# Performance work log

Hardware: AMD Instinct MI355X
Metric: run time of the kernel (lower is better)

## Reference

```python
import jax, jax.numpy as jnp
import numpy as np

B, SQ, SK, H, HK, D = 2, 2048, 2048, 32, 8, 128

def setup_inputs() -> dict:
    key = jax.random.key(0)
    k1, k2, k3 = jax.random.split(key, 3)
    q = jax.random.normal(k1, (B, SQ, H, D), dtype=jnp.float32)
    kv = jax.random.normal(k2, (B, SK, 2, HK, D), dtype=jnp.float32)
    # ragged valid lengths per batch (True = keep)
    lengths = jax.random.randint(k3, (B,), SK // 2, SK + 1)
    key_padding_mask = jnp.arange(SK)[None, :] < lengths[:, None]
    return {"q": q, "kv": kv, "key_padding_mask": key_padding_mask}

def reference(q, kv, key_padding_mask):
    b, sq, h, d = q.shape
    sk, hk = kv.shape[1], kv.shape[3]
    if hk != h:
        kv = jnp.repeat(kv, h // hk, axis=3)  # GQA: (hkv g) contiguous repeat
    k, v = kv[:, :, 0], kv[:, :, 1]  # (B, Sk, H, D)
    scale = 1.0 / jnp.sqrt(jnp.asarray(d, dtype=q.dtype))
    scores = jnp.einsum('bthd,bshd->bhts', q, k * scale)  # (B, H, Sq, Sk)
    pad = jnp.where(key_padding_mask, 0.0, -10000.0).astype(scores.dtype)
    scores = scores + pad[:, None, None, :]
    row = jnp.arange(sq)[:, None]
    col = jnp.arange(sk)[None, :]
    sk_valid = key_padding_mask.sum(-1)[:, None, None, None]  # (B,1,1,1)
    causal_mask = col[None, None] > row[None, None] + sk_valid - sq
    scores = jnp.where(causal_mask, jnp.asarray(-10000.0, scores.dtype), scores)
    attention = jax.nn.softmax(scores, axis=-1)
    # dropout p=0.0 -> identity
    return jnp.einsum('bhts,bshd->bthd', attention, v)  # (B, Sq, H, D)
```

## Files before the change

### kernel.cpp

```cpp
#include <hip/hip_runtime.h>
#include <hip/hip_bf16.h>
#include <cstdint>
#include <cstddef>

constexpr int B_ = 2, SQ_ = 2048, SK_ = 2048, H_ = 32, HK_ = 8, D_ = 128;
constexpr float SCALE_ = 0.08838834764831845f;

typedef __attribute__((ext_vector_type(4))) float f32x4;
typedef __attribute__((ext_vector_type(8))) short bf16x8;
typedef __attribute__((ext_vector_type(4))) short bf16x4;

__device__ __forceinline__ unsigned short f2bf(float f) {
  union { float f; uint32_t u; } v; v.f = f;
  uint32_t u = v.u;
  return (unsigned short)((u + 0x7FFFu + ((u >> 16) & 1u)) >> 16);
}

__device__ __forceinline__ void gload16(const void* g, void* l) {
  __builtin_amdgcn_global_load_lds((const __attribute__((address_space(1))) void*)g,
                                   (__attribute__((address_space(3))) void*)l, 16, 0, 0);
}

__device__ __forceinline__ f32x4 mfma_k16(bf16x4 a, bf16x4 b, f32x4 c) {
#if __has_builtin(__builtin_amdgcn_mfma_f32_16x16x16bf16_1k)
  return __builtin_amdgcn_mfma_f32_16x16x16bf16_1k(a, b, c, 0, 0, 0);
#else
  bf16x8 a8 = {a[0], a[1], a[2], a[3], 0, 0, 0, 0};
  bf16x8 b8 = {b[0], b[1], b[2], b[3], 0, 0, 0, 0};
  return __builtin_amdgcn_mfma_f32_16x16x32_bf16(a8, b8, c, 0, 0, 0);
#endif
}

__global__ void skv_kernel(const void* __restrict__ mask, int* __restrict__ skv_out) {
  const int b = blockIdx.x;
  const int tid = threadIdx.x;
  __shared__ int red[256];
  const uint32_t* mw = (const uint32_t*)mask;
  const uint32_t w0 = mw[0], w1 = mw[1];
  int cnt = 0;
  if (w0 > 1u) {
    const uint8_t* m = (const uint8_t*)mask + (size_t)b * SK_;
    for (int s = tid; s < SK_; s += 256) cnt += (m[s] != 0);
  } else if (w1 == 0u) {
    const uint32_t* m = mw + (size_t)b * SK_ * 2;
    for (int s = tid; s < SK_; s += 256) cnt += (m[2 * s] != 0);
  } else {
    const int* m = (const int*)mask + (size_t)b * SK_;
    for (int s = tid; s < SK_; s += 256) cnt += (m[s] != 0);
  }
  red[tid] = cnt;
  __syncthreads();
  for (int o = 128; o > 0; o >>= 1) {
    if (tid < o) red[tid] += red[tid + o];
    __syncthreads();
  }
  if (tid == 0) skv_out[b] = red[0];
}

__global__ void meanv_kernel(const float* __restrict__ kv, float* __restrict__ meanv) {
  const int blk = blockIdx.x;
  const int chunk = blk & 15;
  const int hk = (blk >> 4) & 7;
  const int b = blk >> 7;
  const int d = threadIdx.x;
  float sum = 0.0f;
  for (int i = 0; i < 128; ++i) {
    const int s = chunk * 128 + i;
    sum += kv[((((size_t)b * SK_ + s) * 2 + 1) * HK_ + hk) * D_ + d];
  }
  atomicAdd(meanv + ((size_t)b * HK_ + hk) * D_ + d, sum * (1.0f / (float)SK_));
}

__global__ void convk(const float* __restrict__ kv, unsigned short* __restrict__ Kb) {
  const int b = blockIdx.z, hk = blockIdx.y;
  const int s = blockIdx.x * 16 + (threadIdx.x >> 4);
  const int dc = (threadIdx.x & 15) * 8;
  const float* src = kv + ((((size_t)b * SK_ + s) * 2 + 0) * HK_ + hk) * D_ + dc;
  f32x4 a0 = *(const f32x4*)src;
  f32x4 a1 = *(const f32x4*)(src + 4);
  bf16x8 t;
  t[0] = (short)f2bf(a0[0]); t[1] = (short)f2bf(a0[1]);
  t[2] = (short)f2bf(a0[2]); t[3] = (short)f2bf(a0[3]);
  t[4] = (short)f2bf(a1[0]); t[5] = (short)f2bf(a1[1]);
  t[6] = (short)f2bf(a1[2]); t[7] = (short)f2bf(a1[3]);
  *(bf16x8*)(Kb + ((size_t)(b * HK_ + hk) * SK_ + s) * D_ + dc) = t;
}

__global__ void convvt(const float* __restrict__ kv, unsigned short* __restrict__ VTb) {
  const int b = blockIdx.z, hk = blockIdx.y;
  const int s0 = blockIdx.x * 64;
  const int d = threadIdx.x & 127;
  const int sg = threadIdx.x >> 7;
  unsigned short vals[32];
#pragma unroll
  for (int i = 0; i < 32; ++i) {
    const int s = s0 + sg * 32 + i;
    vals[i] = f2bf(kv[((((size_t)b * SK_ + s) * 2 + 1) * HK_ + hk) * D_ + d]);
  }
  unsigned short* dst = VTb + ((size_t)(b * HK_ + hk) * D_ + d) * SK_ + s0 + sg * 32;
#pragma unroll
  for (int c = 0; c < 4; ++c) {
    bf16x8 t;
#pragma unroll
    for (int i = 0; i < 8; ++i) t[i] = (short)vals[c * 8 + i];
    *(bf16x8*)(dst + c * 8) = t;
  }
}

__global__ __launch_bounds__(256, 2)
void flash10(const float* __restrict__ q, const unsigned short* __restrict__ Kb,
             const unsigned short* __restrict__ VTb, const int* __restrict__ skv_arr,
             const float* __restrict__ meanv, float* __restrict__ out,
             int* __restrict__ work_ctr) {
  const int tid = threadIdx.x;
  const int w = tid >> 6, l = tid & 63, lg = l >> 4, lr = l & 15;

  __shared__ char smem[65536];
  char* kc0 = smem;          char* vc0 = smem + 16384;
  char* kn0 = smem + 32768;  char* vn0 = smem + 49152;

  const int NITEMS = (SQ_ / 32) * HK_ * B_;

  for (;;) {
    if (tid == 0) *(volatile int*)smem = atomicAdd(work_ctr, 1);
    __syncthreads();
    const int r = *(volatile int*)smem;
    __syncthreads();
    if (r >= NITEMS) break;

    const int qt = 63 - (r >> 4);
    const int hk = (r >> 1) & 7;
    const int b = r & 1;
    const int h = hk * 4 + w;
    const int t0 = qt * 32;
    const int skv = skv_arr[b];

    char* kc = kc0; char* kn = kn0; char* vc = vc0; char* vn = vn0;

    bf16x8 qf[2][4];
#pragma unroll
    for (int rb = 0; rb < 2; ++rb) {
      const int trow = t0 + rb * 16 + lr;
      const float* qp = q + (((size_t)b * SQ_ + trow) * H_ + h) * D_;
#pragma unroll
      for (int kk = 0; kk < 4; ++kk) {
        f32x4 a0 = *(const f32x4*)(qp + kk * 32 + lg * 8);
        f32x4 a1 = *(const f32x4*)(qp + kk * 32 + lg * 8 + 4);
        bf16x8 t;
        t[0] = (short)f2bf(a0[0]); t[1] = (short)f2bf(a0[1]);
        t[2] = (short)f2bf(a0[2]); t[3] = (short)f2bf(a0[3]);
        t[4] = (short)f2bf(a1[0]); t[5] = (short)f2bf(a1[1]);
        t[6] = (short)f2bf(a1[2]); t[7] = (short)f2bf(a1[3]);
        qf[rb][kk] = t;
      }
    }

    f32x4 acc0[8], acc1[8];
#pragma unroll
    for (int i = 0; i < 8; ++i) { acc0[i] = (f32x4)0.0f; acc1[i] = (f32x4)0.0f; }
    float m_[2], l_[2];
#pragma unroll
    for (int rb = 0; rb < 2; ++rb) { m_[rb] = -1e30f; l_[rb] = 0.0f; }

    int n_allowed = t0 + 31 + skv - SQ_ + 1;
    if (n_allowed > skv) n_allowed = skv;
    const int nt = (n_allowed > 0) ? ((n_allowed + 63) >> 6) : 0;

    const char* kgb = (const char*)Kb + ((size_t)(b * HK_ + hk)) * SK_ * D_ * 2;
    const char* vgb = (const char*)VTb + ((size_t)(b * HK_ + hk)) * (size_t)D_ * SK_ * 2;

    auto stage = [&](char* kdst, char* vdst, int s0) {
      const char* kt = kgb + (size_t)s0 * 256;
#pragma unroll
      for (int i = 0; i < 4; ++i) {
        const int c8 = w * 4 + i;
        const int beta = c8 * 1024 + l * 16;
        const int row = beta >> 8;
        gload16(kt + (beta ^ ((row & 7) << 4)), kdst + c8 * 1024);
      }
      const char* vt = vgb + s0 * 2;
#pragma unroll
      for (int i = 0; i < 4; ++i) {
        const int c8 = w * 4 + i;
        const int beta = c8 * 1024 + l * 16;
        const int lam = beta ^ (((beta >> 7) & 7) << 4);
        const int d = lam >> 7, keyb = lam & 127;
        gload16(vt + (size_t)d * (SK_ * 2) + keyb, vdst + c8 * 1024);
      }
    };

    asm volatile("s_waitcnt vmcnt(0)" ::: "memory");
    if (nt > 0) stage(kc, vc, 0);

    for (int j = 0; j < nt; ++j) {
      if (j + 1 < nt) {
        stage(kn, vn, (j + 1) * 64);
        asm volatile("s_waitcnt vmcnt(8)" ::: "memory");
      } else {
        asm volatile("s_waitcnt vmcnt(0)" ::: "memory");
      }
      __builtin_amdgcn_s_barrier();

      const int s0 = j * 64;
      f32x4 sc[2][4];
#pragma unroll
      for (int c = 0; c < 4; ++c) { sc[0][c] = (f32x4)0.0f; sc[1][c] = (f32x4)0.0f; }
#pragma unroll
      for (int c = 0; c < 4; ++c) {
        const int row = c * 16 + lr;
        const int kx = (row & 7) << 4;
#pragma unroll
        for (int kk = 0; kk < 4; ++kk) {
          const int byte = (row << 8) + ((kk * 32 + lg * 8) << 1);
          bf16x8 kf = *(const bf16x8*)(kc + (byte ^ kx));
          sc[0][c] = __builtin_amdgcn_mfma_f32_16x16x32_bf16(kf, qf[0][kk], sc[0][c], 0, 0, 0);
          sc[1][c] = __builtin_amdgcn_mfma_f32_16x16x32_bf16(kf, qf[1][kk], sc[1][c], 0, 0, 0);
        }
      }

      const int kbase = s0 + (lg << 2);
      float pmax[2];
#pragma unroll
      for (int rb = 0; rb < 2; ++rb) {
        const int lim = t0 + rb * 16 + lr + skv - SQ_;
        float mx = -1e30f;
#pragma unroll
        for (int c = 0; c < 4; ++c)
#pragma unroll
          for (int rr = 0; rr < 4; ++rr) {
            const int key = kbase + c * 16 + rr;
            float sv = (key <= lim) ? sc[rb][c][rr] * SCALE_ : -1e30f;
            sc[rb][c][rr] = sv;
            mx = fmaxf(mx, sv);
          }
        mx = fmaxf(mx, __shfl_xor(mx, 16));
        mx = fmaxf(mx, __shfl_xor(mx, 32));
        pmax[rb] = mx;
      }

      const float worst = fmaxf(pmax[0] - m_[0], pmax[1] - m_[1]);
      if (!__all(worst <= 8.0f)) {
        float al_[2];
#pragma unroll
        for (int rb = 0; rb < 2; ++rb) {
          const float mn = fmaxf(m_[rb], pmax[rb]);
          al_[rb] = __expf(m_[rb] - mn);
          m_[rb] = mn;
          l_[rb] *= al_[rb];
        }
        float alq0[4], alq1[4];
#pragma unroll
        for (int rr = 0; rr < 4; ++rr) {
          alq0[rr] = __shfl(al_[0], lg * 4 + rr, 16);
          alq1[rr] = __shfl(al_[1], lg * 4 + rr, 16);
        }
#pragma unroll
        for (int dd = 0; dd < 8; ++dd)
#pragma unroll
          for (int rr = 0; rr < 4; ++rr) { acc0[dd][rr] *= alq0[rr]; acc1[dd][rr] *= alq1[rr]; }
      }

#pragma unroll
      for (int rb = 0; rb < 2; ++rb) {
        float ps = 0.0f;
#pragma unroll
        for (int c = 0; c < 4; ++c)
#pragma unroll
          for (int rr = 0; rr < 4; ++rr) {
            const float pv = __expf(sc[rb][c][rr] - m_[rb]);
            sc[rb][c][rr] = pv;
            ps += pv;
          }
        ps += __shfl_xor(ps, 16);
        ps += __shfl_xor(ps, 32);
        l_[rb] += ps;
      }

      bf16x4 pa[2][4];
#pragma unroll
      for (int rb = 0; rb < 2; ++rb)
#pragma unroll
        for (int c = 0; c < 4; ++c) {
          const f32x4 s4 = rb ? sc[1][c] : sc[0][c];
          bf16x4 t;
          t[0] = (short)f2bf(s4[0]); t[1] = (short)f2bf(s4[1]);
          t[2] = (short)f2bf(s4[2]); t[3] = (short)f2bf(s4[3]);
          pa[rb][c] = t;
        }

#pragma unroll
      for (int dd = 0; dd < 8; ++dd) {
        const int d = dd * 16 + lr;
#pragma unroll
        for (int c = 0; c < 4; ++c) {
          const int lam = d * 128 + c * 32 + lg * 8;
          bf16x4 vf = *(const bf16x4*)(vc + (lam ^ ((d & 7) << 4)));
          acc0[dd] = mfma_k16(pa[0][c], vf, acc0[dd]);
          acc1[dd] = mfma_k16(pa[1][c], vf, acc1[dd]);
        }
      }
      asm volatile("" ::: "memory");
      __builtin_amdgcn_s_barrier();
      { char* t = kc; kc = kn; kn = t; t = vc; vc = vn; vn = t; }
    }

    const float* mp = meanv + ((size_t)(b * HK_ + hk)) * D_;
#pragma unroll
    for (int rb = 0; rb < 2; ++rb) {
      const f32x4* acc = rb ? acc1 : acc0;
      const float lsrc = rb ? l_[1] : l_[0];
#pragma unroll
      for (int rr = 0; rr < 4; ++rr) {
        const float lq = __shfl(lsrc, lg * 4 + rr, 16);
        const int t_r = t0 + rb * 16 + lg * 4 + rr;
        const bool deg = (t_r + skv - SQ_) < 0;
        const float inv = 1.0f / lq;
        float* op = out + (((size_t)b * SQ_ + t_r) * H_ + h) * D_;
#pragma unroll
        for (int dd = 0; dd < 8; ++dd) {
          const int d = dd * 16 + lr;
          op[d] = deg ? mp[d] : acc[dd][rr] * inv;
        }
      }
    }
    __syncthreads();
  }
}

extern "C" void kernel_launch(void* const* d_in, const int* in_sizes, int n_in,
                              void* d_out, int out_size, void* d_ws, size_t ws_size,
                              hipStream_t stream) {
  const float* q = (const float*)d_in[0];
  const float* kv = (const float*)d_in[1];
  const void* mask = d_in[2];
  float* out = (float*)d_out;

  const size_t KB_OFF = 0;
  const size_t VT_OFF = 8ull * 1024 * 1024;
  const size_t MV_OFF = 16ull * 1024 * 1024;
  unsigned short* Kb = (unsigned short*)((char*)d_ws + KB_OFF);
  unsigned short* VTb = (unsigned short*)((char*)d_ws + VT_OFF);
  float* meanv = (float*)((char*)d_ws + MV_OFF);
  int* skv = (int*)((char*)d_ws + MV_OFF + 8192);
  int* work_ctr = (int*)((char*)d_ws + MV_OFF + 8192 + 64);

  hipMemsetAsync((char*)d_ws + MV_OFF, 0, 8192 + 128, stream);
  skv_kernel<<<B_, 256, 0, stream>>>(mask, skv);
  convk<<<dim3(SK_ / 16, HK_, B_), 256, 0, stream>>>(kv, Kb);
  convvt<<<dim3(SK_ / 64, HK_, B_), 256, 0, stream>>>(kv, VTb);
  meanv_kernel<<<B_ * HK_ * 16, 128, 0, stream>>>(kv, meanv);
  flash10<<<dim3(512), 256, 0, stream>>>(q, Kb, VTb, skv, meanv, out, work_ctr);
}
```

Baseline: 182.8 us.

## Split each query tile across two waves per head using 512-thread blocks

Each block now runs 8 waves instead of 4. Each pair of waves shares a head and splits the 32 query rows into two 16-row halves, so every wave holds half the accumulators and score registers. Staging loads are spread across twice as many waves. The intent is to raise occupancy and latency hiding by cutting per-wave register pressure, at the cost of each wave re-reading K/V fragments from LDS for fewer rows, which doubles LDS read traffic per query row.

Result: slower. 228.9 us (+25.3%).

```diff
diff --git a/kernel.cpp b/kernel.cpp
--- a/kernel.cpp
+++ b/kernel.cpp
@@ -107,13 +107,15 @@
   }
 }
 
-__global__ __launch_bounds__(256, 2)
-void flash10(const float* __restrict__ q, const unsigned short* __restrict__ Kb,
+__global__ __launch_bounds__(512, 4)
+void flash11(const float* __restrict__ q, const unsigned short* __restrict__ Kb,
              const unsigned short* __restrict__ VTb, const int* __restrict__ skv_arr,
              const float* __restrict__ meanv, float* __restrict__ out,
              int* __restrict__ work_ctr) {
   const int tid = threadIdx.x;
   const int w = tid >> 6, l = tid & 63, lg = l >> 4, lr = l & 15;
+  const int hd = w >> 1;
+  const int qh = w & 1;
 
   __shared__ char smem[65536];
   char* kc0 = smem;          char* vc0 = smem + 16384;
@@ -131,16 +133,15 @@
     const int qt = 63 - (r >> 4);
     const int hk = (r >> 1) & 7;
     const int b = r & 1;
-    const int h = hk * 4 + w;
+    const int h = hk * 4 + hd;
     const int t0 = qt * 32;
     const int skv = skv_arr[b];
 
     char* kc = kc0; char* kn = kn0; char* vc = vc0; char* vn = vn0;
 
-    bf16x8 qf[2][4];
-#pragma unroll
-    for (int rb = 0; rb < 2; ++rb) {
-      const int trow = t0 + rb * 16 + lr;
+    bf16x8 qf[4];
+    {
+      const int trow = t0 + qh * 16 + lr;
       const float* qp = q + (((size_t)b * SQ_ + trow) * H_ + h) * D_;
 #pragma unroll
       for (int kk = 0; kk < 4; ++kk) {
@@ -151,16 +152,14 @@
         t[2] = (short)f2bf(a0[2]); t[3] = (short)f2bf(a0[3]);
         t[4] = (short)f2bf(a1[0]); t[5] = (short)f2bf(a1[1]);
         t[6] = (short)f2bf(a1[2]); t[7] = (short)f2bf(a1[3]);
-        qf[rb][kk] = t;
+        qf[kk] = t;
       }
     }
 
-    f32x4 acc0[8], acc1[8];
-#pragma unroll
-    for (int i = 0; i < 8; ++i) { acc0[i] = (f32x4)0.0f; acc1[i] = (f32x4)0.0f; }
-    float m_[2], l_[2];
-#pragma unroll
-    for (int rb = 0; rb < 2; ++rb) { m_[rb] = -1e30f; l_[rb] = 0.0f; }
+    f32x4 acc[8];
+#pragma unroll
+    for (int i = 0; i < 8; ++i) acc[i] = (f32x4)0.0f;
+    float m_ = -1e30f, l_ = 0.0f;
 
     int n_allowed = t0 + 31 + skv - SQ_ + 1;
     if (n_allowed > skv) n_allowed = skv;
@@ -172,16 +171,16 @@
     auto stage = [&](char* kdst, char* vdst, int s0) {
       const char* kt = kgb + (size_t)s0 * 256;
 #pragma unroll
-      for (int i = 0; i < 4; ++i) {
-        const int c8 = w * 4 + i;
+      for (int i = 0; i < 2; ++i) {
+        const int c8 = w * 2 + i;
         const int beta = c8 * 1024 + l * 16;
         const int row = beta >> 8;
         gload16(kt + (beta ^ ((row & 7) << 4)), kdst + c8 * 1024);
       }
       const char* vt = vgb + s0 * 2;
 #pragma unroll
-      for (int i = 0; i < 4; ++i) {
-        const int c8 = w * 4 + i;
+      for (int i = 0; i < 2; ++i) {
+        const int c8 = w * 2 + i;
         const int beta = c8 * 1024 + l * 16;
         const int lam = beta ^ (((beta >> 7) & 7) << 4);
         const int d = lam >> 7, keyb = lam & 127;
@@ -195,16 +194,16 @@
     for (int j = 0; j < nt; ++j) {
       if (j + 1 < nt) {
         stage(kn, vn, (j + 1) * 64);
-        asm volatile("s_waitcnt vmcnt(8)" ::: "memory");
+        asm volatile("s_waitcnt vmcnt(4)" ::: "memory");
       } else {
         asm volatile("s_waitcnt vmcnt(0)" ::: "memory");
       }
       __builtin_amdgcn_s_barrier();
 
       const int s0 = j * 64;
-      f32x4 sc[2][4];
-#pragma unroll
-      for (int c = 0; c < 4; ++c) { sc[0][c] = (f32x4)0.0f; sc[1][c] = (f32x4)0.0f; }
+      f32x4 sc[4];
+#pragma unroll
+      for (int c = 0; c < 4; ++c) sc[c] = (f32x4)0.0f;
 #pragma unroll
       for (int c = 0; c < 4; ++c) {
         const int row = c * 16 + lr;
@@ -213,80 +212,62 @@
         for (int kk = 0; kk < 4; ++kk) {
           const int byte = (row << 8) + ((kk * 32 + lg * 8) << 1);
           bf16x8 kf = *(const bf16x8*)(kc + (byte ^ kx));
-          sc[0][c] = __builtin_amdgcn_mfma_f32_16x16x32_bf16(kf, qf[0][kk], sc[0][c], 0, 0, 0);
-          sc[1][c] = __builtin_amdgcn_mfma_f32_16x16x32_bf16(kf, qf[1][kk], sc[1][c], 0, 0, 0);
+          sc[c] = __builtin_amdgcn_mfma_f32_16x16x32_bf16(kf, qf[kk], sc[c], 0, 0, 0);
         }
       }
 
       const int kbase = s0 + (lg << 2);
-      float pmax[2];
-#pragma unroll
-      for (int rb = 0; rb < 2; ++rb) {
-        const int lim = t0 + rb * 16 + lr + skv - SQ_;
-        float mx = -1e30f;
+      const int lim = t0 + qh * 16 + lr + skv - SQ_;
+      float pmax = -1e30f;
+#pragma unroll
+      for (int c = 0; c < 4; ++c)
+#pragma unroll
+        for (int rr = 0; rr < 4; ++rr) {
+          const int key = kbase + c * 16 + rr;
+          float sv = (key <= lim) ? sc[c][rr] * SCALE_ : -1e30f;
+          sc[c][rr] = sv;
+          pmax = fmaxf(pmax, sv);
+        }
+      pmax = fmaxf(pmax, __shfl_xor(pmax, 16));
+      pmax = fmaxf(pmax, __shfl_xor(pmax, 32));
+
+      if (!__all(pmax - m_ <= 8.0f)) {
+        const float mn = fmaxf(m_, pmax);
+        const float al = __expf(m_ - mn);
+        m_ = mn;
+        l_ *= al;
+        float alq[4];
+#pragma unroll
+        for (int rr = 0; rr < 4; ++rr) alq[rr] = __shfl(al, lg * 4 + rr, 16);
+#pragma unroll
+        for (int dd = 0; dd < 8; ++dd)
+#pragma unroll
+          for (int rr = 0; rr < 4; ++rr) acc[dd][rr] *= alq[rr];
+      }
+
+      {
+        float ps = 0.0f;
 #pragma unroll
         for (int c = 0; c < 4; ++c)
 #pragma unroll
           for (int rr = 0; rr < 4; ++rr) {
-            const int key = kbase + c * 16 + rr;
-            float sv = (key <= lim) ? sc[rb][c][rr] * SCALE_ : -1e30f;
-            sc[rb][c][rr] = sv;
-            mx = fmaxf(mx, sv);
-          }
-        mx = fmaxf(mx, __shfl_xor(mx, 16));
-        mx = fmaxf(mx, __shfl_xor(mx, 32));
-        pmax[rb] = mx;
-      }
-
-      const float worst = fmaxf(pmax[0] - m_[0], pmax[1] - m_[1]);
-      if (!__all(worst <= 8.0f)) {
-        float al_[2];
-#pragma unroll
-        for (int rb = 0; rb < 2; ++rb) {
-          const float mn = fmaxf(m_[rb], pmax[rb]);
-          al_[rb] = __expf(m_[rb] - mn);
-          m_[rb] = mn;
-          l_[rb] *= al_[rb];
-        }
-        float alq0[4], alq1[4];
-#pragma unroll
-        for (int rr = 0; rr < 4; ++rr) {
-          alq0[rr] = __shfl(al_[0], lg * 4 + rr, 16);
-          alq1[rr] = __shfl(al_[1], lg * 4 + rr, 16);
-        }
-#pragma unroll
-        for (int dd = 0; dd < 8; ++dd)
-#pragma unroll
-          for (int rr = 0; rr < 4; ++rr) { acc0[dd][rr] *= alq0[rr]; acc1[dd][rr] *= alq1[rr]; }
-      }
-
-#pragma unroll
-      for (int rb = 0; rb < 2; ++rb) {
-        float ps = 0.0f;
-#pragma unroll
-        for (int c = 0; c < 4; ++c)
-#pragma unroll
-          for (int rr = 0; rr < 4; ++rr) {
-            const float pv = __expf(sc[rb][c][rr] - m_[rb]);
-            sc[rb][c][rr] = pv;
+            const float pv = __expf(sc[c][rr] - m_);
+            sc[c][rr] = pv;
             ps += pv;
           }
         ps += __shfl_xor(ps, 16);
         ps += __shfl_xor(ps, 32);
-        l_[rb] += ps;
-      }
-
-      bf16x4 pa[2][4];
-#pragma unroll
-      for (int rb = 0; rb < 2; ++rb)
-#pragma unroll
-        for (int c = 0; c < 4; ++c) {
-          const f32x4 s4 = rb ? sc[1][c] : sc[0][c];
-          bf16x4 t;
-          t[0] = (short)f2bf(s4[0]); t[1] = (short)f2bf(s4[1]);
-          t[2] = (short)f2bf(s4[2]); t[3] = (short)f2bf(s4[3]);
-          pa[rb][c] = t;
-        }
+        l_ += ps;
+      }
+
+      bf16x4 pa[4];
+#pragma unroll
+      for (int c = 0; c < 4; ++c) {
+        bf16x4 t;
+        t[0] = (short)f2bf(sc[c][0]); t[1] = (short)f2bf(sc[c][1]);
+        t[2] = (short)f2bf(sc[c][2]); t[3] = (short)f2bf(sc[c][3]);
+        pa[c] = t;
+      }
 
 #pragma unroll
       for (int dd = 0; dd < 8; ++dd) {
@@ -295,8 +276,7 @@
         for (int c = 0; c < 4; ++c) {
           const int lam = d * 128 + c * 32 + lg * 8;
           bf16x4 vf = *(const bf16x4*)(vc + (lam ^ ((d & 7) << 4)));
-          acc0[dd] = mfma_k16(pa[0][c], vf, acc0[dd]);
-          acc1[dd] = mfma_k16(pa[1][c], vf, acc1[dd]);
+          acc[dd] = mfma_k16(pa[c], vf, acc[dd]);
         }
       }
       asm volatile("" ::: "memory");
@@ -306,21 +286,16 @@
 
     const float* mp = meanv + ((size_t)(b * HK_ + hk)) * D_;
 #pragma unroll
-    for (int rb = 0; rb < 2; ++rb) {
-      const f32x4* acc = rb ? acc1 : acc0;
-      const float lsrc = rb ? l_[1] : l_[0];
-#pragma unroll
-      for (int rr = 0; rr < 4; ++rr) {
-        const float lq = __shfl(lsrc, lg * 4 + rr, 16);
-        const int t_r = t0 + rb * 16 + lg * 4 + rr;
-        const bool deg = (t_r + skv - SQ_) < 0;
-        const float inv = 1.0f / lq;
-        float* op = out + (((size_t)b * SQ_ + t_r) * H_ + h) * D_;
-#pragma unroll
-        for (int dd = 0; dd < 8; ++dd) {
-          const int d = dd * 16 + lr;
-          op[d] = deg ? mp[d] : acc[dd][rr] * inv;
-        }
+    for (int rr = 0; rr < 4; ++rr) {
+      const float lq = __shfl(l_, lg * 4 + rr, 16);
+      const int t_r = t0 + qh * 16 + lg * 4 + rr;
+      const bool deg = (t_r + skv - SQ_) < 0;
+      const float inv = 1.0f / lq;
+      float* op = out + (((size_t)b * SQ_ + t_r) * H_ + h) * D_;
+#pragma unroll
+      for (int dd = 0; dd < 8; ++dd) {
+        const int d = dd * 16 + lr;
+        op[d] = deg ? mp[d] : acc[dd][rr] * inv;
       }
     }
     __syncthreads();
@@ -349,5 +324,5 @@
   convk<<<dim3(SK_ / 16, HK_, B_), 256, 0, stream>>>(kv, Kb);
   convvt<<<dim3(SK_ / 64, HK_, B_), 256, 0, stream>>>(kv, VTb);
   meanv_kernel<<<B_ * HK_ * 16, 128, 0, stream>>>(kv, meanv);
-  flash10<<<dim3(512), 256, 0, stream>>>(q, Kb, VTb, skv, meanv, out, work_ctr);
-}
+  flash11<<<dim3(512), 512, 0, stream>>>(q, Kb, VTb, skv, meanv, out, work_ctr);
+}
```

## Fold softmax scale into Q with exp2, skip masking on full tiles, defer row-sum reduction

Applied to the files above, without the earlier changes.

Folds the softmax scale and log2(e) into Q at load time, so the inner loop can use the raw v_exp_f32 (exp2) and drop a per-element multiply. Causal masking is applied only to tiles that cross the diagonal. The row-max shuffle reduction now runs only when the lazy rescale threshold is exceeded, and the per-row sum reduction moves out of the loop to the epilogue. It also fuses the bf16 conversion of P into the exp loop and raises wave priority around the MFMA blocks. The changes reduce VALU and cross-lane work per tile, at the risk of precision drift from the larger rescale threshold and the pre-scaled bf16 Q.

New measurement: 167.3 us. 8.4% less time.

```diff
diff --git a/kernel.cpp b/kernel.cpp
--- a/kernel.cpp
+++ b/kernel.cpp
@@ -5,6 +5,8 @@
 
 constexpr int B_ = 2, SQ_ = 2048, SK_ = 2048, H_ = 32, HK_ = 8, D_ = 128;
 constexpr float SCALE_ = 0.08838834764831845f;
+constexpr float QSCALE_ = 0.12751874f;
+constexpr float THR_ = 11.5f;
 
 typedef __attribute__((ext_vector_type(4))) float f32x4;
 typedef __attribute__((ext_vector_type(8))) short bf16x8;
@@ -14,6 +16,17 @@
   union { float f; uint32_t u; } v; v.f = f;
   uint32_t u = v.u;
   return (unsigned short)((u + 0x7FFFu + ((u >> 16) & 1u)) >> 16);
+}
+
+__device__ __forceinline__ unsigned short cvt_bf16(float x) {
+  __hip_bfloat16 h = __float2bfloat16(x);
+  return *reinterpret_cast<unsigned short*>(&h);
+}
+
+__device__ __forceinline__ float exp2_fast(float x) {
+  float r;
+  asm volatile("v_exp_f32 %0, %1" : "=v"(r) : "v"(x));
+  return r;
 }
 
 __device__ __forceinline__ void gload16(const void* g, void* l) {
@@ -108,7 +121,7 @@
 }
 
 __global__ __launch_bounds__(256, 2)
-void flash10(const float* __restrict__ q, const unsigned short* __restrict__ Kb,
+void flash13(const float* __restrict__ q, const unsigned short* __restrict__ Kb,
              const unsigned short* __restrict__ VTb, const int* __restrict__ skv_arr,
              const float* __restrict__ meanv, float* __restrict__ out,
              int* __restrict__ work_ctr) {
@@ -147,10 +160,10 @@
         f32x4 a0 = *(const f32x4*)(qp + kk * 32 + lg * 8);
         f32x4 a1 = *(const f32x4*)(qp + kk * 32 + lg * 8 + 4);
         bf16x8 t;
-        t[0] = (short)f2bf(a0[0]); t[1] = (short)f2bf(a0[1]);
-        t[2] = (short)f2bf(a0[2]); t[3] = (short)f2bf(a0[3]);
-        t[4] = (short)f2bf(a1[0]); t[5] = (short)f2bf(a1[1]);
-        t[6] = (short)f2bf(a1[2]); t[7] = (short)f2bf(a1[3]);
+        t[0] = (short)f2bf(a0[0] * QSCALE_); t[1] = (short)f2bf(a0[1] * QSCALE_);
+        t[2] = (short)f2bf(a0[2] * QSCALE_); t[3] = (short)f2bf(a0[3] * QSCALE_);
+        t[4] = (short)f2bf(a1[0] * QSCALE_); t[5] = (short)f2bf(a1[1] * QSCALE_);
+        t[6] = (short)f2bf(a1[2] * QSCALE_); t[7] = (short)f2bf(a1[3] * QSCALE_);
         qf[rb][kk] = t;
       }
     }
@@ -205,6 +218,7 @@
       f32x4 sc[2][4];
 #pragma unroll
       for (int c = 0; c < 4; ++c) { sc[0][c] = (f32x4)0.0f; sc[1][c] = (f32x4)0.0f; }
+      __builtin_amdgcn_s_setprio(1);
 #pragma unroll
       for (int c = 0; c < 4; ++c) {
         const int row = c * 16 + lr;
@@ -217,34 +231,40 @@
           sc[1][c] = __builtin_amdgcn_mfma_f32_16x16x32_bf16(kf, qf[1][kk], sc[1][c], 0, 0, 0);
         }
       }
+      __builtin_amdgcn_s_setprio(0);
 
       const int kbase = s0 + (lg << 2);
-      float pmax[2];
 #pragma unroll
       for (int rb = 0; rb < 2; ++rb) {
-        const int lim = t0 + rb * 16 + lr + skv - SQ_;
-        float mx = -1e30f;
-#pragma unroll
-        for (int c = 0; c < 4; ++c)
-#pragma unroll
-          for (int rr = 0; rr < 4; ++rr) {
-            const int key = kbase + c * 16 + rr;
-            float sv = (key <= lim) ? sc[rb][c][rr] * SCALE_ : -1e30f;
-            sc[rb][c][rr] = sv;
-            mx = fmaxf(mx, sv);
-          }
-        mx = fmaxf(mx, __shfl_xor(mx, 16));
-        mx = fmaxf(mx, __shfl_xor(mx, 32));
-        pmax[rb] = mx;
-      }
-
-      const float worst = fmaxf(pmax[0] - m_[0], pmax[1] - m_[1]);
-      if (!__all(worst <= 8.0f)) {
+        const int lim_min = t0 + rb * 16 + skv - SQ_;
+        if (s0 + 63 > lim_min) {
+          const int lim = t0 + rb * 16 + lr + skv - SQ_;
+#pragma unroll
+          for (int c = 0; c < 4; ++c)
+#pragma unroll
+            for (int rr = 0; rr < 4; ++rr)
+              if (kbase + c * 16 + rr > lim) sc[rb][c][rr] = -1e30f;
+        }
+      }
+
+      float mx0 = sc[0][0][0], mx1 = sc[1][0][0];
+#pragma unroll
+      for (int c = 0; c < 4; ++c)
+#pragma unroll
+        for (int rr = 0; rr < 4; ++rr) {
+          mx0 = fmaxf(mx0, sc[0][c][rr]);
+          mx1 = fmaxf(mx1, sc[1][c][rr]);
+        }
+      const float worst = fmaxf(mx0 - m_[0], mx1 - m_[1]);
+      if (!__all(worst <= THR_)) {
+        float fm[2] = {mx0, mx1};
         float al_[2];
 #pragma unroll
         for (int rb = 0; rb < 2; ++rb) {
-          const float mn = fmaxf(m_[rb], pmax[rb]);
-          al_[rb] = __expf(m_[rb] - mn);
+          float t = fmaxf(fm[rb], __shfl_xor(fm[rb], 16));
+          t = fmaxf(t, __shfl_xor(t, 32));
+          const float mn = fmaxf(m_[rb], t);
+          al_[rb] = exp2_fast(m_[rb] - mn);
           m_[rb] = mn;
           l_[rb] *= al_[rb];
         }
@@ -260,34 +280,26 @@
           for (int rr = 0; rr < 4; ++rr) { acc0[dd][rr] *= alq0[rr]; acc1[dd][rr] *= alq1[rr]; }
       }
 
+      bf16x4 pa[2][4];
 #pragma unroll
       for (int rb = 0; rb < 2; ++rb) {
+        const float mm = m_[rb];
         float ps = 0.0f;
 #pragma unroll
-        for (int c = 0; c < 4; ++c)
+        for (int c = 0; c < 4; ++c) {
+          bf16x4 t;
 #pragma unroll
           for (int rr = 0; rr < 4; ++rr) {
-            const float pv = __expf(sc[rb][c][rr] - m_[rb]);
-            sc[rb][c][rr] = pv;
+            const float pv = exp2_fast(sc[rb][c][rr] - mm);
             ps += pv;
+            t[rr] = (short)cvt_bf16(pv);
           }
-        ps += __shfl_xor(ps, 16);
-        ps += __shfl_xor(ps, 32);
+          pa[rb][c] = t;
+        }
         l_[rb] += ps;
       }
 
-      bf16x4 pa[2][4];
-#pragma unroll
-      for (int rb = 0; rb < 2; ++rb)
-#pragma unroll
-        for (int c = 0; c < 4; ++c) {
-          const f32x4 s4 = rb ? sc[1][c] : sc[0][c];
-          bf16x4 t;
-          t[0] = (short)f2bf(s4[0]); t[1] = (short)f2bf(s4[1]);
-          t[2] = (short)f2bf(s4[2]); t[3] = (short)f2bf(s4[3]);
-          pa[rb][c] = t;
-        }
-
+      __builtin_amdgcn_s_setprio(1);
 #pragma unroll
       for (int dd = 0; dd < 8; ++dd) {
         const int d = dd * 16 + lr;
@@ -299,6 +311,7 @@
           acc1[dd] = mfma_k16(pa[1][c], vf, acc1[dd]);
         }
       }
+      __builtin_amdgcn_s_setprio(0);
       asm volatile("" ::: "memory");
       __builtin_amdgcn_s_barrier();
       { char* t = kc; kc = kn; kn = t; t = vc; vc = vn; vn = t; }
@@ -308,10 +321,11 @@
 #pragma unroll
     for (int rb = 0; rb < 2; ++rb) {
       const f32x4* acc = rb ? acc1 : acc0;
-      const float lsrc = rb ? l_[1] : l_[0];
+      float lsum = l_[rb] + __shfl_xor(l_[rb], 16);
+      lsum += __shfl_xor(lsum, 32);
 #pragma unroll
       for (int rr = 0; rr < 4; ++rr) {
-        const float lq = __shfl(lsrc, lg * 4 + rr, 16);
+        const float lq = __shfl(lsum, lg * 4 + rr, 16);
         const int t_r = t0 + rb * 16 + lg * 4 + rr;
         const bool deg = (t_r + skv - SQ_) < 0;
         const float inv = 1.0f / lq;
@@ -349,5 +363,5 @@
   convk<<<dim3(SK_ / 16, HK_, B_), 256, 0, stream>>>(kv, Kb);
   convvt<<<dim3(SK_ / 64, HK_, B_), 256, 0, stream>>>(kv, VTb);
   meanv_kernel<<<B_ * HK_ * 16, 128, 0, stream>>>(kv, meanv);
-  flash10<<<dim3(512), 256, 0, stream>>>(q, Kb, VTb, skv, meanv, out, work_ctr);
-}
+  flash13<<<dim3(512), 256, 0, stream>>>(q, Kb, VTb, skv, meanv, out, work_ctr);
+}
```
